# Performance work log

Measured on AMD Instinct MI355X. Metric: run time of the kernel, lower is better.

The kernel has to match this reference:

```python
import jax, jax.numpy as jnp
import numpy as np

N = 50000          # masked node count
E = 800000         # edges (avg degree 16)
IN_DIM, GCN_DIM, REL_DIM, TRAIN_DIM, OUT_DIM = 3, 128, 64, 128, 2
BATCHES = 1


def setup_inputs() -> dict:
    key = jax.random.key(0)
    ks = jax.random.split(key, 16)
    s = 0.05
    return {
        "features": jax.random.normal(ks[0], (N, IN_DIM), jnp.float32),
        "edge_index": jax.random.randint(ks[1], (2, E), 0, N, dtype=jnp.int32),
        "trainOT": jax.random.normal(ks[2], (TRAIN_DIM,), jnp.float32),
        "W1": jax.random.normal(ks[3], (IN_DIM, GCN_DIM), jnp.float32) * s,
        "b1": jnp.zeros((GCN_DIM,), jnp.float32),
        "W2": jax.random.normal(ks[4], (GCN_DIM, GCN_DIM), jnp.float32) * s,
        "b2": jnp.zeros((GCN_DIM,), jnp.float32),
        "Wq": jax.random.normal(ks[5], (GCN_DIM, REL_DIM), jnp.float32) * s,
        "bq": jnp.zeros((REL_DIM,), jnp.float32),
        "Wk": jax.random.normal(ks[6], (TRAIN_DIM, REL_DIM), jnp.float32) * s,
        "bk": jnp.zeros((REL_DIM,), jnp.float32),
        "Wv": jax.random.normal(ks[7], (GCN_DIM, TRAIN_DIM), jnp.float32) * s,
        "bv": jnp.zeros((TRAIN_DIM,), jnp.float32),
        "Ws": jax.random.normal(ks[8], (TRAIN_DIM, OUT_DIM * N), jnp.float32) * s,
        "bs": jnp.zeros((OUT_DIM * N,), jnp.float32),
    }


def _gcn_conv(x, W, b, src, dst, n):
    """PyG GCNConv: h = D^-1/2 (A+I) D^-1/2 (x W) + b (self-loops already in src/dst)."""
    h = x @ W                                                  # [n, d_out]
    ones = jnp.ones(src.shape[0], dtype=x.dtype)
    deg = jax.ops.segment_sum(ones, dst, num_segments=n)      # in-degree incl. self-loop
    dinv = jnp.where(deg > 0, jax.lax.rsqrt(deg), 0.0)
    norm = dinv[src] * dinv[dst]                               # [E+n]
    msg = h[src] * norm[:, None]                               # gather (dominant traffic)
    return jax.ops.segment_sum(msg, dst, num_segments=n) + b   # scatter-add


def reference(features, edge_index, trainOT, W1, b1, W2, b2, Wq, bq, Wk, bk, Wv, bv, Ws, bs):
    n = features.shape[0]
    loop = jnp.arange(n, dtype=edge_index.dtype)
    src = jnp.concatenate([edge_index[0], loop])
    dst = jnp.concatenate([edge_index[1], loop])

    h1 = jax.nn.relu(_gcn_conv(features, W1, b1, src, dst, n))   # gcn1 + relu
    h2 = _gcn_conv(h1, W2, b2, src, dst, n)                      # gcn2

    q = h2 @ Wq + bq                                             # [n, rel]
    v = h2 @ Wv + bv                                             # [n, train]
    k = trainOT @ Wk + bk                                        # [rel]
    scale = jnp.asarray(Wq.shape[1], q.dtype) ** 0.5
    rel = jax.nn.sigmoid((q @ k) / scale)                        # [n]
    summed_idea = (rel[:, None] * v).sum(axis=0)                 # [train]
    new_trainOT = trainOT + summed_idea
    speak = new_trainOT @ Ws + bs                                # [out_dim * num_nodes]
    out = speak.reshape(BATCHES, -1, OUT_DIM)
    return out, new_trainOT
```

## Files before the change

kernel.cpp:

```cpp
#include <hip/hip_runtime.h>
#include <math.h>

#define O_RPD    (0)
#define O_RPS    (256*1024)
#define O_DINV   (512*1024)
#define O_SMALL  (768*1024)
#define O_Y      (1024*1024)
#define O_RELW   (1280*1024)
#define O_REL    (1536*1024)
#define O_GHD    (1792*1024)
#define O_GHS    (2048*1024)
#define O_GOD    (2304*1024)
#define O_GOS    (2560*1024)
#define O_BSD    (2816*1024)
#define O_BSS    (2944*1024)
#define O_PART   (3072*1024)
#define O_XS     (3712*1024)
#define O_G1     (4608*1024)
#define O_SRTD   (5632*1024)
#define O_SRTS   (9216*1024)
#define O_COLD   (12544*1024)
#define O_COLS   (16128*1024)

#define NCHUNK 256
#define ZBLOCKS 1024

static __device__ __forceinline__ int blockExclScan256(int v, volatile int* lds, int t) {
    int lane = t & 63, wid = t >> 6;
    int incl = v;
#pragma unroll
    for (int off = 1; off < 64; off <<= 1) {
        int n = __shfl_up(incl, off);
        if (lane >= off) incl += n;
    }
    if (lane == 63) lds[wid] = incl;
    __syncthreads();
    if (t == 0) {
        int s = 0;
#pragma unroll
        for (int i = 0; i < 4; ++i) { int x = lds[i]; lds[i] = s; s += x; }
    }
    __syncthreads();
    return lds[wid] + incl - v;
}

__global__ void k_hist(const int* __restrict__ eidx, int* __restrict__ ghD,
                       int* __restrict__ ghS, int E, int CS, int NB) {
    __shared__ int lh[256];
    int b = blockIdx.x, t = threadIdx.x;
    const int* arr = blockIdx.y ? eidx : (eidx + E);
    int* gh = blockIdx.y ? ghS : ghD;
    lh[t] = 0; __syncthreads();
    int s = b * CS, e = min(E, s + CS);
    for (int i = s + t; i < e; i += 256) atomicAdd(&lh[arr[i] >> 8], 1);
    __syncthreads();
    if (t < NB) gh[t * NCHUNK + b] = lh[t];
}

__global__ void k_bstart(const int* __restrict__ ghD, const int* __restrict__ ghS,
                         int* __restrict__ bsD, int* __restrict__ bsS, int NB) {
    __shared__ int lds1[4];
    __shared__ int lds2[4];
    int t = threadIdx.x;
    int vD = 0, vS = 0;
    if (t < NB) {
        const int* rD = ghD + t * NCHUNK;
        const int* rS = ghS + t * NCHUNK;
        for (int b = 0; b < NCHUNK; ++b) { vD += rD[b]; vS += rS[b]; }
    }
    int exD = blockExclScan256(vD, lds1, t);
    if (t <= NB) bsD[t] = exD;
    __syncthreads();
    int exS = blockExclScan256(vS, lds2, t);
    if (t <= NB) bsS[t] = exS;
}

__global__ void k_goff(const int* __restrict__ ghD, const int* __restrict__ ghS,
                       const int* __restrict__ bsD, const int* __restrict__ bsS,
                       int* __restrict__ goD, int* __restrict__ goS, int NB) {
    __shared__ int lds1[4];
    int nb = blockIdx.x, t = threadIdx.x;
    const int* gh = blockIdx.y ? ghS : ghD;
    const int* bs = blockIdx.y ? bsS : bsD;
    int* go = blockIdx.y ? goS : goD;
    int base = bs[nb];
    int g = gh[nb * NCHUNK + t];
    int gx = blockExclScan256(g, lds1, t);
    go[nb * NCHUNK + t] = base + gx;
}

__global__ void k_scatter(const int* __restrict__ eidx, const int* __restrict__ goD,
                          const int* __restrict__ goS, unsigned int* __restrict__ srtD,
                          unsigned int* __restrict__ srtS, int E, int CS, int NB) {
    __shared__ int lcur[256];
    int b = blockIdx.x, t = threadIdx.x;
    const int* key = blockIdx.y ? eidx : (eidx + E);
    const int* val = blockIdx.y ? (eidx + E) : eidx;
    const int* go  = blockIdx.y ? goS : goD;
    unsigned int* srt = blockIdx.y ? srtS : srtD;
    if (t < NB) lcur[t] = go[t * NCHUNK + b];
    __syncthreads();
    int s = b * CS, e = min(E, s + CS);
    for (int i = s + t; i < e; i += 256) {
        int k = key[i];
        int pos = atomicAdd(&lcur[k >> 8], 1);
        srt[pos] = ((unsigned int)(k & 255) << 16) | (unsigned int)val[i];
    }
}

__global__ void k_build(const unsigned int* __restrict__ srtD, const unsigned int* __restrict__ srtS,
                        const int* __restrict__ bsD, const int* __restrict__ bsS,
                        int* __restrict__ rpD, int* __restrict__ rpS,
                        int* __restrict__ colD, int* __restrict__ colS,
                        float* __restrict__ dinv, const float* __restrict__ x,
                        float4* __restrict__ xs4, const float* __restrict__ bs,
                        float* __restrict__ out, int N, int NB) {
    __shared__ int lcnt[256];
    __shared__ int lpos[256];
    __shared__ int lds1[4];
    int nb = blockIdx.x, t = threadIdx.x;
    bool rev = blockIdx.y != 0;
    const unsigned int* srt = rev ? srtS : srtD;
    const int* bst = rev ? bsS : bsD;
    int* rp  = rev ? rpS : rpD;
    int* col = rev ? colS : colD;
    lcnt[t] = 0; __syncthreads();
    int s = bst[nb], e = bst[nb + 1];
    for (int i = s + t; i < e; i += 256) atomicAdd(&lcnt[srt[i] >> 16], 1);
    __syncthreads();
    int c = lcnt[t];
    int cx = blockExclScan256(c, lds1, t);
    int rpv = s + cx;
    int node = (nb << 8) + t;
    rp[node] = rpv;
    lpos[t] = rpv;
    if (!rev && node < N) {
        float d = rsqrtf((float)(c + 1));
        dinv[node] = d;
        float4 v;
        v.x = x[node * 3] * d; v.y = x[node * 3 + 1] * d; v.z = x[node * 3 + 2] * d; v.w = 0.f;
        xs4[node] = v;
        reinterpret_cast<float2*>(out)[node] = reinterpret_cast<const float2*>(bs)[node];
    }
    __syncthreads();
    for (int i = s + t; i < e; i += 256) {
        unsigned int v = srt[i];
        int p = atomicAdd(&lpos[v >> 16], 1);
        col[p] = (int)(v & 0xffffu);
    }
}

__global__ void k_tiny1(const float* __restrict__ trainOT, const float* __restrict__ Wq,
                        const float* __restrict__ bq, const float* __restrict__ Wk,
                        const float* __restrict__ bk, const float* __restrict__ W2,
                        const float* __restrict__ b2, float* __restrict__ small) {
    __shared__ float kv[64];
    __shared__ float wqk[128];
    __shared__ float red[128];
    int t = threadIdx.x;
    if (t < 64) {
        float acc = bk[t];
        for (int j = 0; j < 128; ++j) acc += trainOT[j] * Wk[j * 64 + t];
        kv[t] = acc;
    }
    __syncthreads();
    float accq = 0.f;
    for (int c = 0; c < 64; ++c) accq += Wq[t * 64 + c] * kv[c];
    wqk[t] = accq;
    red[t] = (t < 64) ? bq[t] * kv[t] : 0.f;
    __syncthreads();
    for (int off = 64; off >= 1; off >>= 1) { if (t < off) red[t] += red[t + off]; __syncthreads(); }
    float bqs = red[0];
    __syncthreads();
    float acc2 = 0.f;
    for (int j = 0; j < 128; ++j) acc2 += W2[t * 128 + j] * wqk[j];
    small[t] = acc2;
    red[t] = b2[t] * wqk[t];
    __syncthreads();
    for (int off = 64; off >= 1; off >>= 1) { if (t < off) red[t] += red[t + off]; __syncthreads(); }
    if (t == 0) small[128] = bqs + red[0];
}

__global__ void k_y(const float4* __restrict__ xs4, const int* __restrict__ rpD,
                    const int* __restrict__ colD, const float* __restrict__ dinv,
                    const float* __restrict__ W1, const float* __restrict__ b1,
                    const float* __restrict__ small, float4* __restrict__ g1,
                    float* __restrict__ y, int N) {
    int t = threadIdx.x;
    int sub = t & 15;
    int node = blockIdx.x * 16 + (t >> 4);
    if (node >= N) return;
    float di = dinv[node];
    int s = rpD[node], e = rpD[node + 1];
    float a0 = 0.f, a1 = 0.f, a2 = 0.f;
    for (int j = s + sub; j < e; j += 16) {
        float4 xv = xs4[colD[j]];
        a0 += xv.x; a1 += xv.y; a2 += xv.z;
    }
    if (sub == 0) { float4 xv = xs4[node]; a0 += xv.x; a1 += xv.y; a2 += xv.z; }
#pragma unroll
    for (int off = 1; off < 16; off <<= 1) {
        a0 += __shfl_xor(a0, off);
        a1 += __shfl_xor(a1, off);
        a2 += __shfl_xor(a2, off);
    }
    a0 *= di; a1 *= di; a2 *= di;
    float yl = 0.f;
#pragma unroll
    for (int m = 0; m < 8; ++m) {
        int c = sub * 8 + m;
        float h = fmaxf(a0 * W1[c] + a1 * W1[128 + c] + a2 * W1[256 + c] + b1[c], 0.f);
        yl += h * small[c];
    }
#pragma unroll
    for (int off = 1; off < 16; off <<= 1) yl += __shfl_xor(yl, off);
    if (sub == 0) {
        y[node] = yl * di;
        float4 gv; gv.x = a0; gv.y = a1; gv.z = a2; gv.w = di;
        g1[node] = gv;
    }
}

__global__ void k_dv(const float* __restrict__ y, const int* __restrict__ rpD,
                     const int* __restrict__ colD, const float* __restrict__ dinv,
                     const float* __restrict__ small, float* __restrict__ relw,
                     float* __restrict__ rel, int N) {
    int t = threadIdx.x;
    int sub = t & 15;
    int node = blockIdx.x * 16 + (t >> 4);
    if (node >= N) return;
    float di = dinv[node];
    int s = rpD[node], e = rpD[node + 1];
    float acc = (sub == 0) ? y[node] : 0.f;
    for (int j = s + sub; j < e; j += 16) acc += y[colD[j]];
#pragma unroll
    for (int off = 1; off < 16; off <<= 1) acc += __shfl_xor(acc, off);
    float z = (acc * di + small[128]) * 0.125f;
    float r = 1.f / (1.f + __expf(-z));
    if (sub == 0) { rel[node] = r; relw[node] = r * di; }
}

__global__ void k_z(const float4* __restrict__ g1, const int* __restrict__ rpS,
                    const int* __restrict__ colS, const float* __restrict__ relw,
                    const float* __restrict__ rel, const float* __restrict__ W1,
                    const float* __restrict__ b1, float* __restrict__ part, int N) {
    __shared__ float W1s[384];
    __shared__ float b1s[128];
    __shared__ float sS[4][132];
    int t = threadIdx.x, lane = t & 63, wid = t >> 6;
    int sub = lane & 15;
    if (t < 128) { W1s[t] = W1[t]; W1s[128 + t] = W1[128 + t]; W1s[256 + t] = W1[256 + t];
                   b1s[t] = b1[t]; }
    __syncthreads();
    float acc[8];
#pragma unroll
    for (int m = 0; m < 8; ++m) acc[m] = 0.f;
    float Racc = 0.f;
    for (int node = blockIdx.x * 16 + (t >> 4); node < N; node += ZBLOCKS * 16) {
        int s = rpS[node], e = rpS[node + 1];
        float w = (sub == 0) ? relw[node] : 0.f;
        for (int j = s + sub; j < e; j += 16) w += relw[colS[j]];
#pragma unroll
        for (int off = 1; off < 16; off <<= 1) w += __shfl_xor(w, off);
        float4 gv = g1[node];
        float zw = w * gv.w;
#pragma unroll
        for (int m = 0; m < 8; ++m) {
            int c = sub * 8 + m;
            float h = fmaxf(gv.x * W1s[c] + gv.y * W1s[128 + c] + gv.z * W1s[256 + c] + b1s[c], 0.f);
            acc[m] += zw * h;
        }
        if (sub == 0) Racc += rel[node];
    }
#pragma unroll
    for (int m = 0; m < 8; ++m) {
        acc[m] += __shfl_xor(acc[m], 16);
        acc[m] += __shfl_xor(acc[m], 32);
    }
    Racc += __shfl_xor(Racc, 16);
    Racc += __shfl_xor(Racc, 32);
    if (lane < 16) {
#pragma unroll
        for (int m = 0; m < 8; ++m) sS[wid][sub * 8 + m] = acc[m];
    }
    if (lane == 0) sS[wid][128] = Racc;
    __syncthreads();
    if (t < 129) part[blockIdx.x * 132 + t] = sS[0][t] + sS[1][t] + sS[2][t] + sS[3][t];
}

__global__ void k_reduce_part(const float* __restrict__ part, int nblocks, float* __restrict__ small) {
    int c = blockIdx.x;
    float acc = 0.f;
    for (int b = threadIdx.x; b < nblocks; b += blockDim.x) acc += part[b * 132 + c];
    __shared__ float sd[256];
    sd[threadIdx.x] = acc; __syncthreads();
    for (int off = 128; off; off >>= 1) { if (threadIdx.x < off) sd[threadIdx.x] += sd[threadIdx.x + off]; __syncthreads(); }
    if (threadIdx.x == 0) small[132 + c] = sd[0];
}

__global__ void k_tinytail(const float* __restrict__ trainOT, const float* __restrict__ W2,
                           const float* __restrict__ b2, const float* __restrict__ Wv,
                           const float* __restrict__ bv, float* __restrict__ small,
                           float* __restrict__ out_tail) {
    __shared__ float partial[1024];
    __shared__ float Ss[128];
    __shared__ float t1[128];
    int t = threadIdx.x;
    int o = t & 127, sl = t >> 7;
    if (t < 128) Ss[t] = small[132 + t];
    __syncthreads();
    float R = small[260];
    float acc = 0.f;
#pragma unroll
    for (int j = sl * 16; j < sl * 16 + 16; ++j) acc += Ss[j] * W2[j * 128 + o];
    partial[t] = acc; __syncthreads();
    if (t < 128) {
        float v = R * b2[t];
#pragma unroll
        for (int k = 0; k < 8; ++k) v += partial[t + 128 * k];
        t1[t] = v;
    }
    __syncthreads();
    float acc2 = 0.f;
#pragma unroll
    for (int j = sl * 16; j < sl * 16 + 16; ++j) acc2 += t1[j] * Wv[j * 128 + o];
    partial[t] = acc2; __syncthreads();
    if (t < 128) {
        float v = R * bv[t];
#pragma unroll
        for (int k = 0; k < 8; ++k) v += partial[t + 128 * k];
        float nt = trainOT[t] + v;
        small[264 + t] = nt;
        out_tail[t] = nt;
    }
}

__global__ void k_tail(const float* __restrict__ Ws, const float* __restrict__ small,
                       float* __restrict__ out, int out_n) {
    int ks = blockIdx.x & 3;
    int j = ((blockIdx.x >> 2) << 8) + threadIdx.x;
    if (j >= out_n) return;
    const float* w = Ws + (size_t)(ks * 32) * out_n + j;
    const float* nt = small + 264 + ks * 32;
    float acc = 0.f;
#pragma unroll 8
    for (int k = 0; k < 32; ++k) acc += nt[k] * w[(size_t)k * out_n];
    atomicAdd(&out[j], acc);
}

extern "C" void kernel_launch(void* const* d_in, const int* in_sizes, int n_in,
                              void* d_out, int out_size, void* d_ws, size_t ws_size,
                              hipStream_t stream) {
    const float* features = (const float*)d_in[0];
    const int*   eidx     = (const int*)d_in[1];
    const float* trainOT  = (const float*)d_in[2];
    const float* W1 = (const float*)d_in[3];
    const float* b1 = (const float*)d_in[4];
    const float* W2 = (const float*)d_in[5];
    const float* b2 = (const float*)d_in[6];
    const float* Wq = (const float*)d_in[7];
    const float* bq = (const float*)d_in[8];
    const float* Wk = (const float*)d_in[9];
    const float* bk = (const float*)d_in[10];
    const float* Wv = (const float*)d_in[11];
    const float* bv = (const float*)d_in[12];
    const float* Ws = (const float*)d_in[13];
    const float* bs = (const float*)d_in[14];

    int N = in_sizes[0] / 3;
    int E = in_sizes[1] / 2;
    int NB = (N + 255) >> 8;
    int CS = (E + NCHUNK - 1) / NCHUNK;

    char* ws = (char*)d_ws;
    int*   rpD   = (int*)(ws + O_RPD);
    int*   rpS   = (int*)(ws + O_RPS);
    float* dinv  = (float*)(ws + O_DINV);
    float* small = (float*)(ws + O_SMALL);
    float* y     = (float*)(ws + O_Y);
    float* relw  = (float*)(ws + O_RELW);
    float* rel   = (float*)(ws + O_REL);
    int*   ghD   = (int*)(ws + O_GHD);
    int*   ghS   = (int*)(ws + O_GHS);
    int*   goD   = (int*)(ws + O_GOD);
    int*   goS   = (int*)(ws + O_GOS);
    int*   bsD   = (int*)(ws + O_BSD);
    int*   bsS   = (int*)(ws + O_BSS);
    float* part  = (float*)(ws + O_PART);
    float4* xs4  = (float4*)(ws + O_XS);
    float4* g1   = (float4*)(ws + O_G1);
    unsigned int* srtD = (unsigned int*)(ws + O_SRTD);
    unsigned int* srtS = (unsigned int*)(ws + O_SRTS);
    int*   colD  = (int*)(ws + O_COLD);
    int*   colS  = (int*)(ws + O_COLS);
    float* out   = (float*)d_out;
    int out_n = out_size - 128;

    k_tiny1<<<1, 128, 0, stream>>>(trainOT, Wq, bq, Wk, bk, W2, b2, small);
    k_hist<<<dim3(NCHUNK, 2), 256, 0, stream>>>(eidx, ghD, ghS, E, CS, NB);
    k_bstart<<<1, 256, 0, stream>>>(ghD, ghS, bsD, bsS, NB);
    k_goff<<<dim3(NB, 2), 256, 0, stream>>>(ghD, ghS, bsD, bsS, goD, goS, NB);
    k_scatter<<<dim3(NCHUNK, 2), 256, 0, stream>>>(eidx, goD, goS, srtD, srtS, E, CS, NB);
    k_build<<<dim3(NB, 2), 256, 0, stream>>>(srtD, srtS, bsD, bsS, rpD, rpS, colD, colS,
                                             dinv, features, xs4, bs, out, N, NB);
    k_y<<<(N + 15) / 16, 256, 0, stream>>>(xs4, rpD, colD, dinv, W1, b1, small, g1, y, N);
    k_dv<<<(N + 15) / 16, 256, 0, stream>>>(y, rpD, colD, dinv, small, relw, rel, N);
    k_z<<<ZBLOCKS, 256, 0, stream>>>(g1, rpS, colS, relw, rel, W1, b1, part, N);
    k_reduce_part<<<129, 256, 0, stream>>>(part, ZBLOCKS, small);
    k_tinytail<<<1, 1024, 0, stream>>>(trainOT, W2, b2, Wv, bv, small, out + out_n);
    k_tail<<<((out_n + 255) / 256) * 4, 256, 0, stream>>>(Ws, small, out, out_n);
}
```

Baseline: 108.7 us.

## Cut kernel launches by fusing bucket-start, tiny precompute, reduction and speak bias

Removes the k_bstart, k_tiny1 and k_reduce_part launches. Bucket-start sums now happen inside k_goff, which also runs the tiny Wq·k precompute in one extra block. The partial reduction is folded into the single-block tail kernel, and ZBLOCKS drops from 1024 to 256 so there are fewer partials. The final speak GEMV now does an in-block split-K reduction with float2 loads and adds the bias directly, replacing the atomicAdd onto a bias-initialised output. The trade-offs are redundant per-block row sums in k_goff, less parallelism in k_z, and a doubled histogram chunk count.

```diff
diff --git a/kernel.cpp b/kernel.cpp
--- a/kernel.cpp
+++ b/kernel.cpp
@@ -1,31 +1,31 @@
 #include <hip/hip_runtime.h>
 #include <math.h>
 
-#define O_RPD    (0)
-#define O_RPS    (256*1024)
-#define O_DINV   (512*1024)
-#define O_SMALL  (768*1024)
+#define O_SMALL  (0)
+#define O_RPD    (256*1024)
+#define O_RPS    (512*1024)
+#define O_DINV   (768*1024)
 #define O_Y      (1024*1024)
 #define O_RELW   (1280*1024)
 #define O_REL    (1536*1024)
-#define O_GHD    (1792*1024)
-#define O_GHS    (2048*1024)
-#define O_GOD    (2304*1024)
-#define O_GOS    (2560*1024)
-#define O_BSD    (2816*1024)
-#define O_BSS    (2944*1024)
-#define O_PART   (3072*1024)
-#define O_XS     (3712*1024)
-#define O_G1     (4608*1024)
-#define O_SRTD   (5632*1024)
-#define O_SRTS   (9216*1024)
-#define O_COLD   (12544*1024)
-#define O_COLS   (16128*1024)
-
-#define NCHUNK 256
-#define ZBLOCKS 1024
-
-static __device__ __forceinline__ int blockExclScan256(int v, volatile int* lds, int t) {
+#define O_BSD    (1792*1024)
+#define O_BSS    (1800*1024)
+#define O_PART   (2048*1024)
+#define O_XS     (2816*1024)
+#define O_G1     (3840*1024)
+#define O_GHD    (5120*1024)
+#define O_GHS    (5632*1024)
+#define O_GOD    (6144*1024)
+#define O_GOS    (6656*1024)
+#define O_SRTD   (7168*1024)
+#define O_SRTS   (10496*1024)
+#define O_COLD   (13824*1024)
+#define O_COLS   (17152*1024)
+
+#define NCH 512
+#define ZB  256
+
+static __device__ __forceinline__ int exclScan256(int v, volatile int* lds, int t) {
     int lane = t & 63, wid = t >> 6;
     int incl = v;
 #pragma unroll
@@ -38,7 +38,7 @@
     if (t == 0) {
         int s = 0;
 #pragma unroll
-        for (int i = 0; i < 4; ++i) { int x = lds[i]; lds[i] = s; s += x; }
+        for (int i = 0; i < 4; ++i) { int x2 = lds[i]; lds[i] = s; s += x2; }
     }
     __syncthreads();
     return lds[wid] + incl - v;
@@ -47,60 +47,90 @@
 __global__ void k_hist(const int* __restrict__ eidx, int* __restrict__ ghD,
                        int* __restrict__ ghS, int E, int CS, int NB) {
     __shared__ int lh[256];
-    int b = blockIdx.x, t = threadIdx.x;
+    int c = blockIdx.x, t = threadIdx.x;
     const int* arr = blockIdx.y ? eidx : (eidx + E);
     int* gh = blockIdx.y ? ghS : ghD;
     lh[t] = 0; __syncthreads();
-    int s = b * CS, e = min(E, s + CS);
+    int s = c * CS, e = min(E, s + CS);
     for (int i = s + t; i < e; i += 256) atomicAdd(&lh[arr[i] >> 8], 1);
     __syncthreads();
-    if (t < NB) gh[t * NCHUNK + b] = lh[t];
-}
-
-__global__ void k_bstart(const int* __restrict__ ghD, const int* __restrict__ ghS,
-                         int* __restrict__ bsD, int* __restrict__ bsS, int NB) {
+    if (t < NB) gh[t * NCH + c] = lh[t];
+}
+
+__global__ void k_goff(const int* __restrict__ ghD, const int* __restrict__ ghS,
+                       int* __restrict__ goD, int* __restrict__ goS,
+                       int* __restrict__ bsD, int* __restrict__ bsS,
+                       const float* __restrict__ trainOT, const float* __restrict__ Wq,
+                       const float* __restrict__ bq, const float* __restrict__ Wk,
+                       const float* __restrict__ bk, const float* __restrict__ W2,
+                       const float* __restrict__ b2, float* __restrict__ small,
+                       int E, int NB) {
+    __shared__ int lred[256];
     __shared__ int lds1[4];
-    __shared__ int lds2[4];
-    int t = threadIdx.x;
-    int vD = 0, vS = 0;
-    if (t < NB) {
-        const int* rD = ghD + t * NCHUNK;
-        const int* rS = ghS + t * NCHUNK;
-        for (int b = 0; b < NCHUNK; ++b) { vD += rD[b]; vS += rS[b]; }
-    }
-    int exD = blockExclScan256(vD, lds1, t);
-    if (t <= NB) bsD[t] = exD;
-    __syncthreads();
-    int exS = blockExclScan256(vS, lds2, t);
-    if (t <= NB) bsS[t] = exS;
-}
-
-__global__ void k_goff(const int* __restrict__ ghD, const int* __restrict__ ghS,
-                       const int* __restrict__ bsD, const int* __restrict__ bsS,
-                       int* __restrict__ goD, int* __restrict__ goS, int NB) {
-    __shared__ int lds1[4];
+    __shared__ float kv[64];
+    __shared__ float wqk[128];
+    __shared__ float fred[256];
     int nb = blockIdx.x, t = threadIdx.x;
+    if (nb == NB) {
+        if (blockIdx.y) return;
+        if (t < 64) {
+            float acc = bk[t];
+            for (int j = 0; j < 128; ++j) acc += trainOT[j] * Wk[j * 64 + t];
+            kv[t] = acc;
+        }
+        __syncthreads();
+        if (t < 128) {
+            float aq = 0.f;
+            for (int c2 = 0; c2 < 64; ++c2) aq += Wq[t * 64 + c2] * kv[c2];
+            wqk[t] = aq;
+        }
+        fred[t] = (t < 64) ? bq[t] * kv[t] : 0.f;
+        __syncthreads();
+        for (int off = 128; off >= 1; off >>= 1) { if (t < off) fred[t] += fred[t + off]; __syncthreads(); }
+        float bqs = fred[0];
+        __syncthreads();
+        if (t < 128) {
+            float a2 = 0.f;
+            for (int j = 0; j < 128; ++j) a2 += W2[t * 128 + j] * wqk[j];
+            small[t] = a2;
+        }
+        fred[t] = (t < 128) ? b2[t] * wqk[t] : 0.f;
+        __syncthreads();
+        for (int off = 128; off >= 1; off >>= 1) { if (t < off) fred[t] += fred[t + off]; __syncthreads(); }
+        if (t == 0) small[128] = bqs + fred[0];
+        return;
+    }
     const int* gh = blockIdx.y ? ghS : ghD;
-    const int* bs = blockIdx.y ? bsS : bsD;
     int* go = blockIdx.y ? goS : goD;
-    int base = bs[nb];
-    int g = gh[nb * NCHUNK + t];
-    int gx = blockExclScan256(g, lds1, t);
-    go[nb * NCHUNK + t] = base + gx;
+    int* bs = blockIdx.y ? bsS : bsD;
+    int rs = 0;
+    if (t < nb) {
+        const int4* row = reinterpret_cast<const int4*>(gh + t * NCH);
+        for (int i = 0; i < NCH / 4; ++i) { int4 p = row[i]; rs += p.x + p.y + p.z + p.w; }
+    }
+    lred[t] = rs; __syncthreads();
+    for (int off = 128; off >= 1; off >>= 1) { if (t < off) lred[t] += lred[t + off]; __syncthreads(); }
+    int base = lred[0];
+    __syncthreads();
+    if (t == 0) { bs[nb] = base; if (nb == NB - 1) bs[NB] = E; }
+    int g0 = gh[nb * NCH + 2 * t], g1 = gh[nb * NCH + 2 * t + 1];
+    int ex = exclScan256(g0 + g1, lds1, t);
+    go[nb * NCH + 2 * t] = base + ex;
+    go[nb * NCH + 2 * t + 1] = base + ex + g0;
 }
 
 __global__ void k_scatter(const int* __restrict__ eidx, const int* __restrict__ goD,
                           const int* __restrict__ goS, unsigned int* __restrict__ srtD,
                           unsigned int* __restrict__ srtS, int E, int CS, int NB) {
     __shared__ int lcur[256];
-    int b = blockIdx.x, t = threadIdx.x;
+    int c = blockIdx.x, t = threadIdx.x;
     const int* key = blockIdx.y ? eidx : (eidx + E);
     const int* val = blockIdx.y ? (eidx + E) : eidx;
     const int* go  = blockIdx.y ? goS : goD;
     unsigned int* srt = blockIdx.y ? srtS : srtD;
-    if (t < NB) lcur[t] = go[t * NCHUNK + b];
-    __syncthreads();
-    int s = b * CS, e = min(E, s + CS);
+    if (t < NB) lcur[t] = go[t * NCH + c];
+    __syncthreads();
+    int s = c * CS, e = min(E, s + CS);
     for (int i = s + t; i < e; i += 256) {
         int k = key[i];
         int pos = atomicAdd(&lcur[k >> 8], 1);
@@ -113,8 +143,7 @@
                         int* __restrict__ rpD, int* __restrict__ rpS,
                         int* __restrict__ colD, int* __restrict__ colS,
                         float* __restrict__ dinv, const float* __restrict__ x,
-                        float4* __restrict__ xs4, const float* __restrict__ bs,
-                        float* __restrict__ out, int N, int NB) {
+                        float4* __restrict__ xs4, int N, int NB) {
     __shared__ int lcnt[256];
     __shared__ int lpos[256];
     __shared__ int lds1[4];
@@ -129,7 +158,7 @@
     for (int i = s + t; i < e; i += 256) atomicAdd(&lcnt[srt[i] >> 16], 1);
     __syncthreads();
     int c = lcnt[t];
-    int cx = blockExclScan256(c, lds1, t);
+    int cx = exclScan256(c, lds1, t);
     int rpv = s + cx;
     int node = (nb << 8) + t;
     rp[node] = rpv;
@@ -140,7 +169,6 @@
         float4 v;
         v.x = x[node * 3] * d; v.y = x[node * 3 + 1] * d; v.z = x[node * 3 + 2] * d; v.w = 0.f;
         xs4[node] = v;
-        reinterpret_cast<float2*>(out)[node] = reinterpret_cast<const float2*>(bs)[node];
     }
     __syncthreads();
     for (int i = s + t; i < e; i += 256) {
@@ -148,37 +176,6 @@
         int p = atomicAdd(&lpos[v >> 16], 1);
         col[p] = (int)(v & 0xffffu);
     }
-}
-
-__global__ void k_tiny1(const float* __restrict__ trainOT, const float* __restrict__ Wq,
-                        const float* __restrict__ bq, const float* __restrict__ Wk,
-                        const float* __restrict__ bk, const float* __restrict__ W2,
-                        const float* __restrict__ b2, float* __restrict__ small) {
-    __shared__ float kv[64];
-    __shared__ float wqk[128];
-    __shared__ float red[128];
-    int t = threadIdx.x;
-    if (t < 64) {
-        float acc = bk[t];
-        for (int j = 0; j < 128; ++j) acc += trainOT[j] * Wk[j * 64 + t];
-        kv[t] = acc;
-    }
-    __syncthreads();
-    float accq = 0.f;
-    for (int c = 0; c < 64; ++c) accq += Wq[t * 64 + c] * kv[c];
-    wqk[t] = accq;
-    red[t] = (t < 64) ? bq[t] * kv[t] : 0.f;
-    __syncthreads();
-    for (int off = 64; off >= 1; off >>= 1) { if (t < off) red[t] += red[t + off]; __syncthreads(); }
-    float bqs = red[0];
-    __syncthreads();
-    float acc2 = 0.f;
-    for (int j = 0; j < 128; ++j) acc2 += W2[t * 128 + j] * wqk[j];
-    small[t] = acc2;
-    red[t] = b2[t] * wqk[t];
-    __syncthreads();
-    for (int off = 64; off >= 1; off >>= 1) { if (t < off) red[t] += red[t + off]; __syncthreads(); }
-    if (t == 0) small[128] = bqs + red[0];
 }
 
 __global__ void k_y(const float4* __restrict__ xs4, const int* __restrict__ rpD,
@@ -256,7 +253,7 @@
 #pragma unroll
     for (int m = 0; m < 8; ++m) acc[m] = 0.f;
     float Racc = 0.f;
-    for (int node = blockIdx.x * 16 + (t >> 4); node < N; node += ZBLOCKS * 16) {
+    for (int node = blockIdx.x * 16 + (t >> 4); node < N; node += ZB * 16) {
         int s = rpS[node], e = rpS[node + 1];
         float w = (sub == 0) ? relw[node] : 0.f;
         for (int j = s + sub; j < e; j += 16) w += relw[colS[j]];
@@ -288,64 +285,83 @@
     if (t < 129) part[blockIdx.x * 132 + t] = sS[0][t] + sS[1][t] + sS[2][t] + sS[3][t];
 }
 
-__global__ void k_reduce_part(const float* __restrict__ part, int nblocks, float* __restrict__ small) {
-    int c = blockIdx.x;
-    float acc = 0.f;
-    for (int b = threadIdx.x; b < nblocks; b += blockDim.x) acc += part[b * 132 + c];
-    __shared__ float sd[256];
-    sd[threadIdx.x] = acc; __syncthreads();
-    for (int off = 128; off; off >>= 1) { if (threadIdx.x < off) sd[threadIdx.x] += sd[threadIdx.x + off]; __syncthreads(); }
-    if (threadIdx.x == 0) small[132 + c] = sd[0];
-}
-
-__global__ void k_tinytail(const float* __restrict__ trainOT, const float* __restrict__ W2,
-                           const float* __restrict__ b2, const float* __restrict__ Wv,
-                           const float* __restrict__ bv, float* __restrict__ small,
-                           float* __restrict__ out_tail) {
-    __shared__ float partial[1024];
-    __shared__ float Ss[128];
+__global__ void k_tailred(const float* __restrict__ trainOT, const float* __restrict__ W2,
+                          const float* __restrict__ b2, const float* __restrict__ Wv,
+                          const float* __restrict__ bv, const float* __restrict__ part,
+                          float* __restrict__ small, float* __restrict__ out_tail) {
+    __shared__ float acc8[1024];
+    __shared__ float Ss[129];
     __shared__ float t1[128];
+    __shared__ float r8[8];
     int t = threadIdx.x;
-    int o = t & 127, sl = t >> 7;
-    if (t < 128) Ss[t] = small[132 + t];
-    __syncthreads();
-    float R = small[260];
-    float acc = 0.f;
-#pragma unroll
-    for (int j = sl * 16; j < sl * 16 + 16; ++j) acc += Ss[j] * W2[j * 128 + o];
-    partial[t] = acc; __syncthreads();
+    int c = t >> 3, sl = t & 7;
+    float s = 0.f;
+    for (int b = sl; b < ZB; b += 8) s += part[b * 132 + c];
+    acc8[t] = s;
+    if (t < 8) {
+        float r = 0.f;
+        for (int b = t; b < ZB; b += 8) r += part[b * 132 + 128];
+        r8[t] = r;
+    }
+    __syncthreads();
+    if (t < 128) {
+        float v = 0.f;
+#pragma unroll
+        for (int k = 0; k < 8; ++k) v += acc8[t * 8 + k];
+        Ss[t] = v;
+    }
+    if (t == 0) Ss[128] = r8[0] + r8[1] + r8[2] + r8[3] + r8[4] + r8[5] + r8[6] + r8[7];
+    __syncthreads();
+    float R = Ss[128];
+    int o = t & 127, s2 = t >> 7;
+    float a1 = 0.f;
+#pragma unroll
+    for (int j = s2 * 16; j < s2 * 16 + 16; ++j) a1 += Ss[j] * W2[j * 128 + o];
+    acc8[t] = a1; __syncthreads();
     if (t < 128) {
         float v = R * b2[t];
 #pragma unroll
-        for (int k = 0; k < 8; ++k) v += partial[t + 128 * k];
+        for (int k = 0; k < 8; ++k) v += acc8[t + 128 * k];
         t1[t] = v;
     }
     __syncthreads();
-    float acc2 = 0.f;
-#pragma unroll
-    for (int j = sl * 16; j < sl * 16 + 16; ++j) acc2 += t1[j] * Wv[j * 128 + o];
-    partial[t] = acc2; __syncthreads();
+    float a2 = 0.f;
+#pragma unroll
+    for (int j = s2 * 16; j < s2 * 16 + 16; ++j) a2 += t1[j] * Wv[j * 128 + o];
+    acc8[t] = a2; __syncthreads();
     if (t < 128) {
         float v = R * bv[t];
 #pragma unroll
-        for (int k = 0; k < 8; ++k) v += partial[t + 128 * k];
+        for (int k = 0; k < 8; ++k) v += acc8[t + 128 * k];
         float nt = trainOT[t] + v;
         small[264 + t] = nt;
         out_tail[t] = nt;
     }
 }
 
-__global__ void k_tail(const float* __restrict__ Ws, const float* __restrict__ small,
-                       float* __restrict__ out, int out_n) {
-    int ks = blockIdx.x & 3;
-    int j = ((blockIdx.x >> 2) << 8) + threadIdx.x;
-    if (j >= out_n) return;
-    const float* w = Ws + (size_t)(ks * 32) * out_n + j;
-    const float* nt = small + 264 + ks * 32;
-    float acc = 0.f;
-#pragma unroll 8
-    for (int k = 0; k < 32; ++k) acc += nt[k] * w[(size_t)k * out_n];
-    atomicAdd(&out[j], acc);
+__global__ void k_speak(const float* __restrict__ Ws, const float* __restrict__ bs,
+                        const float* __restrict__ small, float* __restrict__ out, int out_n) {
+    __shared__ float nt[128];
+    __shared__ float s0[256], s1[256];
+    int t = threadIdx.x;
+    if (t < 128) nt[t] = small[264 + t];
+    __syncthreads();
+    int jj = (t & 63) * 2, sl = t >> 6;
+    int j = blockIdx.x * 128 + jj;
+    float a0 = 0.f, a1 = 0.f;
+    if (j < out_n) {
+        const float* w = Ws + (size_t)(sl * 32) * out_n + j;
+        for (int k = 0; k < 32; ++k) {
+            float cv = nt[sl * 32 + k];
+            float2 r = *reinterpret_cast<const float2*>(w + (size_t)k * out_n);
+            a0 += cv * r.x; a1 += cv * r.y;
+        }
+    }
+    s0[t] = a0; s1[t] = a1; __syncthreads();
+    if (t < 64 && j < out_n) {
+        out[j]     = s0[t] + s0[t + 64] + s0[t + 128] + s0[t + 192] + bs[j];
+        out[j + 1] = s1[t] + s1[t + 64] + s1[t + 128] + s1[t + 192] + bs[j + 1];
+    }
 }
 
 extern "C" void kernel_launch(void* const* d_in, const int* in_sizes, int n_in,
@@ -370,25 +386,25 @@
     int N = in_sizes[0] / 3;
     int E = in_sizes[1] / 2;
     int NB = (N + 255) >> 8;
-    int CS = (E + NCHUNK - 1) / NCHUNK;
+    int CS = (E + NCH - 1) / NCH;
 
     char* ws = (char*)d_ws;
+    float* small = (float*)(ws + O_SMALL);
     int*   rpD   = (int*)(ws + O_RPD);
     int*   rpS   = (int*)(ws + O_RPS);
     float* dinv  = (float*)(ws + O_DINV);
-    float* small = (float*)(ws + O_SMALL);
     float* y     = (float*)(ws + O_Y);
     float* relw  = (float*)(ws + O_RELW);
     float* rel   = (float*)(ws + O_REL);
-    int*   ghD   = (int*)(ws + O_GHD);
-    int*   ghS   = (int*)(ws + O_GHS);
-    int*   goD   = (int*)(ws + O_GOD);
-    int*   goS   = (int*)(ws + O_GOS);
     int*   bsD   = (int*)(ws + O_BSD);
     int*   bsS   = (int*)(ws + O_BSS);
     float* part  = (float*)(ws + O_PART);
     float4* xs4  = (float4*)(ws + O_XS);
     float4* g1   = (float4*)(ws + O_G1);
+    int*   ghD   = (int*)(ws + O_GHD);
+    int*   ghS   = (int*)(ws + O_GHS);
+    int*   goD   = (int*)(ws + O_GOD);
+    int*   goS   = (int*)(ws + O_GOS);
     unsigned int* srtD = (unsigned int*)(ws + O_SRTD);
     unsigned int* srtS = (unsigned int*)(ws + O_SRTS);
     int*   colD  = (int*)(ws + O_COLD);
@@ -396,17 +412,15 @@
     float* out   = (float*)d_out;
     int out_n = out_size - 128;
 
-    k_tiny1<<<1, 128, 0, stream>>>(trainOT, Wq, bq, Wk, bk, W2, b2, small);
-    k_hist<<<dim3(NCHUNK, 2), 256, 0, stream>>>(eidx, ghD, ghS, E, CS, NB);
-    k_bstart<<<1, 256, 0, stream>>>(ghD, ghS, bsD, bsS, NB);
-    k_goff<<<dim3(NB, 2), 256, 0, stream>>>(ghD, ghS, bsD, bsS, goD, goS, NB);
-    k_scatter<<<dim3(NCHUNK, 2), 256, 0, stream>>>(eidx, goD, goS, srtD, srtS, E, CS, NB);
+    k_hist<<<dim3(NCH, 2), 256, 0, stream>>>(eidx, ghD, ghS, E, CS, NB);
+    k_goff<<<dim3(NB + 1, 2), 256, 0, stream>>>(ghD, ghS, goD, goS, bsD, bsS,
+                                                trainOT, Wq, bq, Wk, bk, W2, b2, small, E, NB);
+    k_scatter<<<dim3(NCH, 2), 256, 0, stream>>>(eidx, goD, goS, srtD, srtS, E, CS, NB);
     k_build<<<dim3(NB, 2), 256, 0, stream>>>(srtD, srtS, bsD, bsS, rpD, rpS, colD, colS,
-                                             dinv, features, xs4, bs, out, N, NB);
+                                             dinv, features, xs4, N, NB);
     k_y<<<(N + 15) / 16, 256, 0, stream>>>(xs4, rpD, colD, dinv, W1, b1, small, g1, y, N);
     k_dv<<<(N + 15) / 16, 256, 0, stream>>>(y, rpD, colD, dinv, small, relw, rel, N);
-    k_z<<<ZBLOCKS, 256, 0, stream>>>(g1, rpS, colS, relw, rel, W1, b1, part, N);
-    k_reduce_part<<<129, 256, 0, stream>>>(part, ZBLOCKS, small);
-    k_tinytail<<<1, 1024, 0, stream>>>(trainOT, W2, b2, Wv, bv, small, out + out_n);
-    k_tail<<<((out_n + 255) / 256) * 4, 256, 0, stream>>>(Ws, small, out, out_n);
-}
+    k_z<<<ZB, 256, 0, stream>>>(g1, rpS, colS, relw, rel, W1, b1, part, N);
+    k_tailred<<<1, 1024, 0, stream>>>(trainOT, W2, b2, Wv, bv, part, small, out + out_n);
+    k_speak<<<(out_n + 127) / 128, 256, 0, stream>>>(Ws, bs, small, out, out_n);
+}
```

Result: slower. 125.4 us (+15.4%).
